# Optimization experiments

Hardware: AMD Instinct MI355X
Metric: run time of the kernel (lower is better)

The kernel has to match this reference:

```python
import jax, jax.numpy as jnp
import numpy as np

B, N, IN_DIM, HID, OUT, HEADS = 2, 1024, 64, 64, 64, 4
PHD1, PHD2 = HID // HEADS, OUT // HEADS
SLOPE = 0.2  # PyG GATv2Conv default negative_slope
EPS = 1e-12  # F.normalize eps


def _gatv2_dense(x, Wl, Wr, att, bias, heads, phd, mask):
    """Dense GATv2 layer over a full adjacency mask.
    x: [B,N,Din]; Wl/Wr: [Din, heads*phd]; att: [heads,phd]; bias: [heads*phd];
    mask: [N,N] bool, mask[i,j]=True means edge j->i exists.
    """
    Bb, Nn, _ = x.shape
    xl = (x @ Wl).reshape(Bb, Nn, heads, phd)  # source features
    xr = (x @ Wr).reshape(Bb, Nn, heads, phd)  # target features
    # s[b,i,j,h,p] = leaky_relu(xr[b,i] + xl[b,j])  (GATv2)
    s = jax.nn.leaky_relu(xr[:, :, None] + xl[:, None, :], SLOPE)
    e = jnp.einsum('bijhp,hp->bijh', s, att)  # [B,Ni,Nj,H]
    e = jnp.where(mask[None, :, :, None], e, -jnp.inf)
    alpha = jax.nn.softmax(e, axis=2)  # softmax over source nodes j
    out = jnp.einsum('bijh,bjhp->bihp', alpha, xl).reshape(Bb, Nn, heads * phd)
    return out + bias


def setup_inputs() -> dict:
    key = jax.random.key(0)
    ks = jax.random.split(key, 10)
    sc = 0.1
    return {
        'x': jax.random.normal(ks[0], (B, N, IN_DIM), jnp.float32),
        'embedding': jax.random.normal(ks[1], (N, HID), jnp.float32),
        'Wl1': jax.random.normal(ks[2], (IN_DIM, HEADS * PHD1), jnp.float32) * sc,
        'Wr1': jax.random.normal(ks[3], (IN_DIM, HEADS * PHD1), jnp.float32) * sc,
        'att1': jax.random.normal(ks[4], (HEADS, PHD1), jnp.float32) * sc,
        'b1': jnp.zeros((HEADS * PHD1,), jnp.float32),
        'Wl2': jax.random.normal(ks[5], (HID, HEADS * PHD2), jnp.float32) * sc,
        'Wr2': jax.random.normal(ks[6], (HID, HEADS * PHD2), jnp.float32) * sc,
        'att2': jax.random.normal(ks[7], (HEADS, PHD2), jnp.float32) * sc,
        'b2': jnp.zeros((HEADS * PHD2,), jnp.float32),
    }


def reference(x, embedding, Wl1, Wr1, att1, b1, Wl2, Wr2, att2, b2):
    # AdaptiveAdjacency: cosine-similarity adjacency; only its nonzero pattern is used.
    norm = jnp.maximum(jnp.linalg.norm(embedding, axis=1, keepdims=True), EPS)
    ne = embedding / norm
    adj = ne @ ne.T  # [N,N]
    # edge set = adj.nonzero(); GATv2Conv(add_self_loops=True) guarantees diagonal
    mask = (adj != 0) | jnp.eye(N, dtype=bool)
    h = jax.nn.relu(_gatv2_dense(x, Wl1, Wr1, att1, b1, HEADS, PHD1, mask))
    # dropout(0.3) in eval mode -> identity
    return _gatv2_dense(h, Wl2, Wr2, att2, b2, HEADS, PHD2, mask)
```

## Files before the change

kernel.cpp:

```cpp
#include <hip/hip_runtime.h>
#include <math.h>

#define NN 1024
#define BB 2
#define D 64
#define NHEAD 4
#define PH 16
#define LOG2E 1.4426950408889634f

template <int CTRL>
__device__ __forceinline__ float dpp_mov(float x) {
    int xi = __builtin_bit_cast(int, x);
    int r = __builtin_amdgcn_update_dpp(0, xi, CTRL, 0xF, 0xF, true);
    return __builtin_bit_cast(float, r);
}

__device__ __forceinline__ float dpp_rowsum16(float t) {
    t += dpp_mov<0x111>(t);
    t += dpp_mov<0x112>(t);
    t += dpp_mov<0x114>(t);
    t += dpp_mov<0x118>(t);
    return t;
}

__device__ __forceinline__ float quad_sum4(float t) {
    t += dpp_mov<0xB1>(t);
    t += dpp_mov<0x4E>(t);
    return t;
}

#define MST 65
__global__ __launch_bounds__(256) void k_mask(const float* __restrict__ emb,
                                              unsigned char* __restrict__ mask) {
    __shared__ float As[64 * MST];
    __shared__ float Bs[64 * MST];
    int tid = threadIdx.x;
    int ib = (blockIdx.x & 15) << 6;
    int jb = (blockIdx.x >> 4) << 6;

    #pragma unroll
    for (int r = 0; r < 4; ++r) {
        int q = tid + (r << 8);
        int row = q >> 4, c4 = (q & 15) << 2;
        float4 a = *(const float4*)&emb[(ib + row) * D + c4];
        float4 b = *(const float4*)&emb[(jb + row) * D + c4];
        As[row * MST + c4 + 0] = a.x; As[row * MST + c4 + 1] = a.y;
        As[row * MST + c4 + 2] = a.z; As[row * MST + c4 + 3] = a.w;
        Bs[row * MST + c4 + 0] = b.x; Bs[row * MST + c4 + 1] = b.y;
        Bs[row * MST + c4 + 2] = b.z; Bs[row * MST + c4 + 3] = b.w;
    }
    __syncthreads();

    int i0 = (tid >> 4) << 2;
    int j0 = (tid & 15) << 2;
    float acc[4][4] = {};
    #pragma unroll 8
    for (int k = 0; k < 64; ++k) {
        float a0 = As[(i0 + 0) * MST + k];
        float a1 = As[(i0 + 1) * MST + k];
        float a2 = As[(i0 + 2) * MST + k];
        float a3 = As[(i0 + 3) * MST + k];
        float b0 = Bs[(j0 + 0) * MST + k];
        float b1 = Bs[(j0 + 1) * MST + k];
        float b2 = Bs[(j0 + 2) * MST + k];
        float b3 = Bs[(j0 + 3) * MST + k];
        acc[0][0] = fmaf(a0, b0, acc[0][0]); acc[0][1] = fmaf(a0, b1, acc[0][1]);
        acc[0][2] = fmaf(a0, b2, acc[0][2]); acc[0][3] = fmaf(a0, b3, acc[0][3]);
        acc[1][0] = fmaf(a1, b0, acc[1][0]); acc[1][1] = fmaf(a1, b1, acc[1][1]);
        acc[1][2] = fmaf(a1, b2, acc[1][2]); acc[1][3] = fmaf(a1, b3, acc[1][3]);
        acc[2][0] = fmaf(a2, b0, acc[2][0]); acc[2][1] = fmaf(a2, b1, acc[2][1]);
        acc[2][2] = fmaf(a2, b2, acc[2][2]); acc[2][3] = fmaf(a2, b3, acc[2][3]);
        acc[3][0] = fmaf(a3, b0, acc[3][0]); acc[3][1] = fmaf(a3, b1, acc[3][1]);
        acc[3][2] = fmaf(a3, b2, acc[3][2]); acc[3][3] = fmaf(a3, b3, acc[3][3]);
    }
    #pragma unroll
    for (int r = 0; r < 4; ++r) {
        int gi = ib + i0 + r;
        uchar4 m;
        m.x = (acc[r][0] != 0.f || gi == jb + j0 + 0) ? 1 : 0;
        m.y = (acc[r][1] != 0.f || gi == jb + j0 + 1) ? 1 : 0;
        m.z = (acc[r][2] != 0.f || gi == jb + j0 + 2) ? 1 : 0;
        m.w = (acc[r][3] != 0.f || gi == jb + j0 + 3) ? 1 : 0;
        *(uchar4*)&mask[gi * NN + jb + j0] = m;
    }
}

__global__ __launch_bounds__(256) void k_gemm2(const float* __restrict__ A,
                                               const float* __restrict__ Wl,
                                               const float* __restrict__ Wr,
                                               const float* __restrict__ att,
                                               float* __restrict__ xl,
                                               float* __restrict__ xr,
                                               float* __restrict__ alE) {
    __shared__ float wl[64 * 64];
    __shared__ float wr[64 * 64];
    int tid = threadIdx.x;
    for (int t = tid; t < 4096; t += 256) { wl[t] = Wl[t]; wr[t] = Wr[t]; }
    __syncthreads();
    int r = blockIdx.x * 4 + (tid >> 6);
    int c = tid & 63;
    float av = att[c];
    const float* arow = A + r * 64;
    float accl = 0.f, accr = 0.f;
    #pragma unroll
    for (int p = 0; p < 64; ++p) {
        float a = arow[p];
        accl = fmaf(a, wl[p * 64 + c], accl);
        accr = fmaf(a, wr[p * 64 + c], accr);
    }
    xl[r * 64 + c] = accl;
    xr[r * 64 + c] = accr;
    float t = dpp_rowsum16(accl * av);
    if ((c & 15) == 15) alE[(r << 2) | (c >> 4)] = 0.6f * LOG2E * t;
}

template <bool RELU>
__global__ __launch_bounds__(256, 4) void k_attn(
    const float* __restrict__ xl, const float* __restrict__ xr,
    const float* __restrict__ att, const float* __restrict__ alE,
    const float* __restrict__ bias, const unsigned char* __restrict__ mask,
    float* __restrict__ out)
{
    __shared__ float Opart[2][4][4][64];
    __shared__ float Lpart[2][4][4][NHEAD];

    int tid = threadIdx.x;
    int wave = tid >> 6, lane = tid & 63;
    int h = lane & 3, jl = lane >> 2;
    int b = blockIdx.x >> 9;
    int i0 = (blockIdx.x & 511) << 1;
    int j0 = (wave << 8) + (jl << 4);

    const float* xlb = xl + (b << 16);

    float at[16], xr0f[16], xr1f[16];
    {
        const float* ap = att + (h << 2);
        const float* r0 = xr + (((b << 10) + i0) << 6) + (h << 2);
        const float* r1 = r0 + 64;
        #pragma unroll
        for (int q = 0; q < 4; ++q) {
            *(float4*)&at[q << 2]   = *(const float4*)(ap + (q << 4));
            *(float4*)&xr0f[q << 2] = *(const float4*)(r0 + (q << 4));
            *(float4*)&xr1f[q << 2] = *(const float4*)(r1 + (q << 4));
        }
        #pragma unroll
        for (int p = 0; p < 16; ++p) at[p] *= 0.4f * LOG2E;
    }
    float ar0q[4], ar1q[4];
    #pragma unroll
    for (int q = 0; q < 4; ++q) {
        float p0 = 0.f, p1 = 0.f;
        #pragma unroll
        for (int r = 0; r < 4; ++r) {
            p0 = fmaf(at[(q << 2) + r], xr0f[(q << 2) + r], p0);
            p1 = fmaf(at[(q << 2) + r], xr1f[(q << 2) + r], p1);
        }
        ar0q[q] = 1.5f * quad_sum4(p0);
        ar1q[q] = 1.5f * quad_sum4(p1);
    }

    unsigned mb0 = 0, mb1 = 0;
    {
        const unsigned* m0p = (const unsigned*)(mask + i0 * NN + j0);
        const unsigned* m1p = (const unsigned*)(mask + (i0 + 1) * NN + j0);
        #pragma unroll
        for (int q = 0; q < 4; ++q) {
            unsigned w0 = m0p[q], w1 = m1p[q];
            mb0 |= ((((w0 >> 0) & 1) | ((w0 >> 7) & 2) | ((w0 >> 14) & 4) | ((w0 >> 21) & 8)) << (q << 2));
            mb1 |= ((((w1 >> 0) & 1) | ((w1 >> 7) & 2) | ((w1 >> 14) & 4) | ((w1 >> 21) & 8)) << (q << 2));
        }
    }

    float O0[16], O1[16], l0q[4] = {}, l1q[4] = {};
    #pragma unroll
    for (int p = 0; p < 16; ++p) { O0[p] = 0.f; O1[p] = 0.f; }

    const float* xrow = xlb + (j0 << 6) + (h << 2);
    const float* alp  = alE + (b << 12) + (j0 << 2);

    #pragma unroll 2
    for (int s = 0; s < 16; ++s) {
        const float* rp = xrow + (s << 6);
        float xv[16];
        *(float4*)&xv[0]  = *(const float4*)(rp);
        *(float4*)&xv[4]  = *(const float4*)(rp + 16);
        *(float4*)&xv[8]  = *(const float4*)(rp + 32);
        *(float4*)&xv[12] = *(const float4*)(rp + 48);
        float alr[4];
        *(float4*)alr = *(const float4*)(alp + (s << 2));
        bool m0 = (mb0 >> s) & 1, m1 = (mb1 >> s) & 1;

        #pragma unroll
        for (int q = 0; q < 4; ++q) {
            float p0 = 0.f, p1 = 0.f;
            #pragma unroll
            for (int r = 0; r < 4; ++r) {
                float xvv = xv[(q << 2) + r];
                float a = at[(q << 2) + r];
                p0 = fmaf(a, __builtin_fabsf(xr0f[(q << 2) + r] + xvv), p0);
                p1 = fmaf(a, __builtin_fabsf(xr1f[(q << 2) + r] + xvv), p1);
            }
            float e0 = quad_sum4(p0) + (ar0q[q] + alr[q]);
            float e1 = quad_sum4(p1) + (ar1q[q] + alr[q]);
            float pe0 = m0 ? __builtin_amdgcn_exp2f(e0) : 0.f;
            float pe1 = m1 ? __builtin_amdgcn_exp2f(e1) : 0.f;
            l0q[q] += pe0;
            l1q[q] += pe1;
            #pragma unroll
            for (int r = 0; r < 4; ++r) {
                float xvv = xv[(q << 2) + r];
                O0[(q << 2) + r] = fmaf(pe0, xvv, O0[(q << 2) + r]);
                O1[(q << 2) + r] = fmaf(pe1, xvv, O1[(q << 2) + r]);
            }
        }
    }

    #pragma unroll
    for (int p = 0; p < 16; ++p) {
        O0[p] += dpp_mov<0x114>(O0[p]);  O0[p] += dpp_mov<0x118>(O0[p]);
        O1[p] += dpp_mov<0x114>(O1[p]);  O1[p] += dpp_mov<0x118>(O1[p]);
    }
    #pragma unroll
    for (int q = 0; q < 4; ++q) {
        l0q[q] += dpp_mov<0x114>(l0q[q]);  l0q[q] += dpp_mov<0x118>(l0q[q]);
        l1q[q] += dpp_mov<0x114>(l1q[q]);  l1q[q] += dpp_mov<0x118>(l1q[q]);
    }

    if ((lane & 15) >= 12) {
        int k = lane >> 4;
        #pragma unroll
        for (int q = 0; q < 4; ++q) {
            *(float4*)&Opart[0][wave][k][(q << 4) + (h << 2)] = *(const float4*)&O0[q << 2];
            *(float4*)&Opart[1][wave][k][(q << 4) + (h << 2)] = *(const float4*)&O1[q << 2];
        }
        if (h == 0) {
            #pragma unroll
            for (int q = 0; q < 4; ++q) {
                Lpart[0][wave][k][q] = l0q[q];
                Lpart[1][wave][k][q] = l1q[q];
            }
        }
    }
    __syncthreads();

    if (tid < 128) {
        int ii = tid >> 6, c = tid & 63;
        float o = 0.f, l = 0.f;
        #pragma unroll
        for (int w = 0; w < 4; ++w)
            #pragma unroll
            for (int k = 0; k < 4; ++k) {
                o += Opart[ii][w][k][c];
                l += Lpart[ii][w][k][c >> 4];
            }
        float res = o / l + bias[c];
        if (RELU) res = fmaxf(res, 0.f);
        out[((b << 10) + i0 + ii) * D + c] = res;
    }
}

extern "C" void kernel_launch(void* const* d_in, const int* in_sizes, int n_in,
                              void* d_out, int out_size, void* d_ws, size_t ws_size,
                              hipStream_t stream) {
    const float* x    = (const float*)d_in[0];
    const float* emb  = (const float*)d_in[1];
    const float* Wl1  = (const float*)d_in[2];
    const float* Wr1  = (const float*)d_in[3];
    const float* att1 = (const float*)d_in[4];
    const float* b1   = (const float*)d_in[5];
    const float* Wl2  = (const float*)d_in[6];
    const float* Wr2  = (const float*)d_in[7];
    const float* att2 = (const float*)d_in[8];
    const float* b2   = (const float*)d_in[9];
    float* out = (float*)d_out;

    unsigned char* mask = (unsigned char*)d_ws;
    float* xl = (float*)(mask + NN * NN);
    float* xr = xl + BB * NN * D;
    float* hbuf = xr + BB * NN * D;
    float* alE = hbuf + BB * NN * D;

    k_mask<<<256, 256, 0, stream>>>(emb, mask);

    k_gemm2<<<BB * NN / 4, 256, 0, stream>>>(x, Wl1, Wr1, att1, xl, xr, alE);
    k_attn<true><<<BB * NN / 2, 256, 0, stream>>>(xl, xr, att1, alE, b1, mask, hbuf);

    k_gemm2<<<BB * NN / 4, 256, 0, stream>>>(hbuf, Wl2, Wr2, att2, xl, xr, alE);
    k_attn<false><<<BB * NN / 2, 256, 0, stream>>>(xl, xr, att2, alE, b2, mask, out);
}
```

Measured before the change: 145.2 us.

## Split attention over source halves and fuse mask, projection, and combine kernels

The attention kernel now splits each target-pair's source range into two halves, doubling block count to 2048 and writing partial numerators and denominators to workspace. New kernels merge the two partials, fusing the layer-1 bias and ReLU with the layer-2 projection, and fusing the mask tile computation with the layer-1 projection. The aim is better occupancy and fewer kernel stages. The cost is extra global traffic for the partials, a separate final combine launch, and a per-row projection that leaves most threads idle and reads weights straight from global memory without shared staging.

```diff
diff --git a/kernel.cpp b/kernel.cpp
--- a/kernel.cpp
+++ b/kernel.cpp
@@ -2,10 +2,6 @@
 #include <math.h>
 
 #define NN 1024
-#define BB 2
-#define D 64
-#define NHEAD 4
-#define PH 16
 #define LOG2E 1.4426950408889634f
 
 template <int CTRL>
@@ -14,7 +10,6 @@
     int r = __builtin_amdgcn_update_dpp(0, xi, CTRL, 0xF, 0xF, true);
     return __builtin_bit_cast(float, r);
 }
-
 __device__ __forceinline__ float dpp_rowsum16(float t) {
     t += dpp_mov<0x111>(t);
     t += dpp_mov<0x112>(t);
@@ -22,117 +17,85 @@
     t += dpp_mov<0x118>(t);
     return t;
 }
-
 __device__ __forceinline__ float quad_sum4(float t) {
     t += dpp_mov<0xB1>(t);
     t += dpp_mov<0x4E>(t);
     return t;
 }
 
-#define MST 65
-__global__ __launch_bounds__(256) void k_mask(const float* __restrict__ emb,
-                                              unsigned char* __restrict__ mask) {
-    __shared__ float As[64 * MST];
-    __shared__ float Bs[64 * MST];
+__device__ void mask_tile(const float* __restrict__ emb,
+                          unsigned char* __restrict__ mask, int task, float* sm) {
+    float* As = sm;
+    float* Bs = sm + 32 * 65;
     int tid = threadIdx.x;
-    int ib = (blockIdx.x & 15) << 6;
-    int jb = (blockIdx.x >> 4) << 6;
-
-    #pragma unroll
-    for (int r = 0; r < 4; ++r) {
+    int ib = (task & 31) << 5;
+    int jb = (task >> 5) << 4;
+    #pragma unroll
+    for (int r = 0; r < 2; ++r) {
         int q = tid + (r << 8);
         int row = q >> 4, c4 = (q & 15) << 2;
-        float4 a = *(const float4*)&emb[(ib + row) * D + c4];
-        float4 b = *(const float4*)&emb[(jb + row) * D + c4];
-        As[row * MST + c4 + 0] = a.x; As[row * MST + c4 + 1] = a.y;
-        As[row * MST + c4 + 2] = a.z; As[row * MST + c4 + 3] = a.w;
-        Bs[row * MST + c4 + 0] = b.x; Bs[row * MST + c4 + 1] = b.y;
-        Bs[row * MST + c4 + 2] = b.z; Bs[row * MST + c4 + 3] = b.w;
+        float4 a = *(const float4*)&emb[(ib + row) * 64 + c4];
+        As[row * 65 + c4 + 0] = a.x; As[row * 65 + c4 + 1] = a.y;
+        As[row * 65 + c4 + 2] = a.z; As[row * 65 + c4 + 3] = a.w;
+    }
+    {
+        int row = tid >> 4, c4 = (tid & 15) << 2;
+        float4 b = *(const float4*)&emb[(jb + row) * 64 + c4];
+        Bs[row * 65 + c4 + 0] = b.x; Bs[row * 65 + c4 + 1] = b.y;
+        Bs[row * 65 + c4 + 2] = b.z; Bs[row * 65 + c4 + 3] = b.w;
     }
     __syncthreads();
-
-    int i0 = (tid >> 4) << 2;
-    int j0 = (tid & 15) << 2;
-    float acc[4][4] = {};
+    int i1 = tid >> 4, j = tid & 15;
+    float acc1 = 0.f, acc2 = 0.f;
     #pragma unroll 8
     for (int k = 0; k < 64; ++k) {
-        float a0 = As[(i0 + 0) * MST + k];
-        float a1 = As[(i0 + 1) * MST + k];
-        float a2 = As[(i0 + 2) * MST + k];
-        float a3 = As[(i0 + 3) * MST + k];
-        float b0 = Bs[(j0 + 0) * MST + k];
-        float b1 = Bs[(j0 + 1) * MST + k];
-        float b2 = Bs[(j0 + 2) * MST + k];
-        float b3 = Bs[(j0 + 3) * MST + k];
-        acc[0][0] = fmaf(a0, b0, acc[0][0]); acc[0][1] = fmaf(a0, b1, acc[0][1]);
-        acc[0][2] = fmaf(a0, b2, acc[0][2]); acc[0][3] = fmaf(a0, b3, acc[0][3]);
-        acc[1][0] = fmaf(a1, b0, acc[1][0]); acc[1][1] = fmaf(a1, b1, acc[1][1]);
-        acc[1][2] = fmaf(a1, b2, acc[1][2]); acc[1][3] = fmaf(a1, b3, acc[1][3]);
-        acc[2][0] = fmaf(a2, b0, acc[2][0]); acc[2][1] = fmaf(a2, b1, acc[2][1]);
-        acc[2][2] = fmaf(a2, b2, acc[2][2]); acc[2][3] = fmaf(a2, b3, acc[2][3]);
-        acc[3][0] = fmaf(a3, b0, acc[3][0]); acc[3][1] = fmaf(a3, b1, acc[3][1]);
-        acc[3][2] = fmaf(a3, b2, acc[3][2]); acc[3][3] = fmaf(a3, b3, acc[3][3]);
-    }
-    #pragma unroll
-    for (int r = 0; r < 4; ++r) {
-        int gi = ib + i0 + r;
-        uchar4 m;
-        m.x = (acc[r][0] != 0.f || gi == jb + j0 + 0) ? 1 : 0;
-        m.y = (acc[r][1] != 0.f || gi == jb + j0 + 1) ? 1 : 0;
-        m.z = (acc[r][2] != 0.f || gi == jb + j0 + 2) ? 1 : 0;
-        m.w = (acc[r][3] != 0.f || gi == jb + j0 + 3) ? 1 : 0;
-        *(uchar4*)&mask[gi * NN + jb + j0] = m;
-    }
-}
-
-__global__ __launch_bounds__(256) void k_gemm2(const float* __restrict__ A,
-                                               const float* __restrict__ Wl,
-                                               const float* __restrict__ Wr,
-                                               const float* __restrict__ att,
-                                               float* __restrict__ xl,
-                                               float* __restrict__ xr,
-                                               float* __restrict__ alE) {
-    __shared__ float wl[64 * 64];
-    __shared__ float wr[64 * 64];
+        float bv = Bs[j * 65 + k];
+        acc1 = fmaf(As[i1 * 65 + k], bv, acc1);
+        acc2 = fmaf(As[(i1 + 16) * 65 + k], bv, acc2);
+    }
+    int gi1 = ib + i1, gi2 = ib + i1 + 16, gj = jb + j;
+    mask[gi1 * NN + gj] = (acc1 != 0.f || gi1 == gj) ? 1 : 0;
+    mask[gi2 * NN + gj] = (acc2 != 0.f || gi2 == gj) ? 1 : 0;
+}
+
+__device__ void gemm_row(const float* __restrict__ Wl, const float* __restrict__ Wr,
+                         const float* __restrict__ att, const float* hrow,
+                         float* __restrict__ xl, float* __restrict__ xr,
+                         float* __restrict__ alE, int r) {
     int tid = threadIdx.x;
-    for (int t = tid; t < 4096; t += 256) { wl[t] = Wl[t]; wr[t] = Wr[t]; }
-    __syncthreads();
-    int r = blockIdx.x * 4 + (tid >> 6);
-    int c = tid & 63;
-    float av = att[c];
-    const float* arow = A + r * 64;
-    float accl = 0.f, accr = 0.f;
-    #pragma unroll
-    for (int p = 0; p < 64; ++p) {
-        float a = arow[p];
-        accl = fmaf(a, wl[p * 64 + c], accl);
-        accr = fmaf(a, wr[p * 64 + c], accr);
-    }
-    xl[r * 64 + c] = accl;
-    xr[r * 64 + c] = accr;
-    float t = dpp_rowsum16(accl * av);
-    if ((c & 15) == 15) alE[(r << 2) | (c >> 4)] = 0.6f * LOG2E * t;
-}
-
-template <bool RELU>
-__global__ __launch_bounds__(256, 4) void k_attn(
-    const float* __restrict__ xl, const float* __restrict__ xr,
-    const float* __restrict__ att, const float* __restrict__ alE,
-    const float* __restrict__ bias, const unsigned char* __restrict__ mask,
-    float* __restrict__ out)
-{
-    __shared__ float Opart[2][4][4][64];
-    __shared__ float Lpart[2][4][4][NHEAD];
-
+    if (tid < 64) {
+        int c = tid;
+        float accl = 0.f, accr = 0.f;
+        #pragma unroll 8
+        for (int p = 0; p < 64; ++p) {
+            float a = hrow[p];
+            accl = fmaf(a, Wl[p * 64 + c], accl);
+            accr = fmaf(a, Wr[p * 64 + c], accr);
+        }
+        xl[r * 64 + c] = accl;
+        xr[r * 64 + c] = accr;
+        float t = dpp_rowsum16(accl * att[c]);
+        if ((c & 15) == 15) alE[(r << 2) | (c >> 4)] = 0.6f * LOG2E * t;
+    }
+}
+
+__device__ void attn_partial(const float* __restrict__ xl, const float* __restrict__ xr,
+                             const float* __restrict__ att, const float* __restrict__ alE,
+                             const unsigned char* __restrict__ mask,
+                             float* __restrict__ Opar, float* __restrict__ lpar,
+                             int task, float* sm) {
+    float* sO = sm;
+    float* sL = sm + 2048;
     int tid = threadIdx.x;
     int wave = tid >> 6, lane = tid & 63;
     int h = lane & 3, jl = lane >> 2;
-    int b = blockIdx.x >> 9;
-    int i0 = (blockIdx.x & 511) << 1;
-    int j0 = (wave << 8) + (jl << 4);
+    int js = task & 1;
+    int p  = task >> 1;
+    int b  = p >> 9;
+    int i0 = (p & 511) << 1;
+    int jbase = (js << 9) + (wave << 7) + (jl << 3);
 
     const float* xlb = xl + (b << 16);
-
     float at[16], xr0f[16], xr1f[16];
     {
         const float* ap = att + (h << 2);
@@ -145,42 +108,38 @@
             *(float4*)&xr1f[q << 2] = *(const float4*)(r1 + (q << 4));
         }
         #pragma unroll
-        for (int p = 0; p < 16; ++p) at[p] *= 0.4f * LOG2E;
+        for (int pp = 0; pp < 16; ++pp) at[pp] *= 0.4f * LOG2E;
     }
     float ar0q[4], ar1q[4];
     #pragma unroll
     for (int q = 0; q < 4; ++q) {
         float p0 = 0.f, p1 = 0.f;
         #pragma unroll
-        for (int r = 0; r < 4; ++r) {
-            p0 = fmaf(at[(q << 2) + r], xr0f[(q << 2) + r], p0);
-            p1 = fmaf(at[(q << 2) + r], xr1f[(q << 2) + r], p1);
+        for (int rr = 0; rr < 4; ++rr) {
+            p0 = fmaf(at[(q << 2) + rr], xr0f[(q << 2) + rr], p0);
+            p1 = fmaf(at[(q << 2) + rr], xr1f[(q << 2) + rr], p1);
         }
         ar0q[q] = 1.5f * quad_sum4(p0);
         ar1q[q] = 1.5f * quad_sum4(p1);
     }
-
     unsigned mb0 = 0, mb1 = 0;
     {
-        const unsigned* m0p = (const unsigned*)(mask + i0 * NN + j0);
-        const unsigned* m1p = (const unsigned*)(mask + (i0 + 1) * NN + j0);
-        #pragma unroll
-        for (int q = 0; q < 4; ++q) {
+        const unsigned* m0p = (const unsigned*)(mask + i0 * NN + jbase);
+        const unsigned* m1p = (const unsigned*)(mask + (i0 + 1) * NN + jbase);
+        #pragma unroll
+        for (int q = 0; q < 2; ++q) {
             unsigned w0 = m0p[q], w1 = m1p[q];
             mb0 |= ((((w0 >> 0) & 1) | ((w0 >> 7) & 2) | ((w0 >> 14) & 4) | ((w0 >> 21) & 8)) << (q << 2));
             mb1 |= ((((w1 >> 0) & 1) | ((w1 >> 7) & 2) | ((w1 >> 14) & 4) | ((w1 >> 21) & 8)) << (q << 2));
         }
     }
-
-    float O0[16], O1[16], l0q[4] = {}, l1q[4] = {};
-    #pragma unroll
-    for (int p = 0; p < 16; ++p) { O0[p] = 0.f; O1[p] = 0.f; }
-
-    const float* xrow = xlb + (j0 << 6) + (h << 2);
-    const float* alp  = alE + (b << 12) + (j0 << 2);
-
+    float O0[16], O1[16], l0q[4] = {0,0,0,0}, l1q[4] = {0,0,0,0};
+    #pragma unroll
+    for (int pp = 0; pp < 16; ++pp) { O0[pp] = 0.f; O1[pp] = 0.f; }
+    const float* xrow = xlb + (jbase << 6) + (h << 2);
+    const float* alp  = alE + (b << 12) + (jbase << 2);
     #pragma unroll 2
-    for (int s = 0; s < 16; ++s) {
+    for (int s = 0; s < 8; ++s) {
         const float* rp = xrow + (s << 6);
         float xv[16];
         *(float4*)&xv[0]  = *(const float4*)(rp);
@@ -190,74 +149,135 @@
         float alr[4];
         *(float4*)alr = *(const float4*)(alp + (s << 2));
         bool m0 = (mb0 >> s) & 1, m1 = (mb1 >> s) & 1;
-
         #pragma unroll
         for (int q = 0; q < 4; ++q) {
             float p0 = 0.f, p1 = 0.f;
             #pragma unroll
-            for (int r = 0; r < 4; ++r) {
-                float xvv = xv[(q << 2) + r];
-                float a = at[(q << 2) + r];
-                p0 = fmaf(a, __builtin_fabsf(xr0f[(q << 2) + r] + xvv), p0);
-                p1 = fmaf(a, __builtin_fabsf(xr1f[(q << 2) + r] + xvv), p1);
+            for (int rr = 0; rr < 4; ++rr) {
+                float xvv = xv[(q << 2) + rr];
+                float a = at[(q << 2) + rr];
+                p0 = fmaf(a, __builtin_fabsf(xr0f[(q << 2) + rr] + xvv), p0);
+                p1 = fmaf(a, __builtin_fabsf(xr1f[(q << 2) + rr] + xvv), p1);
             }
             float e0 = quad_sum4(p0) + (ar0q[q] + alr[q]);
             float e1 = quad_sum4(p1) + (ar1q[q] + alr[q]);
             float pe0 = m0 ? __builtin_amdgcn_exp2f(e0) : 0.f;
             float pe1 = m1 ? __builtin_amdgcn_exp2f(e1) : 0.f;
-            l0q[q] += pe0;
-            l1q[q] += pe1;
+            l0q[q] += pe0; l1q[q] += pe1;
             #pragma unroll
-            for (int r = 0; r < 4; ++r) {
-                float xvv = xv[(q << 2) + r];
-                O0[(q << 2) + r] = fmaf(pe0, xvv, O0[(q << 2) + r]);
-                O1[(q << 2) + r] = fmaf(pe1, xvv, O1[(q << 2) + r]);
+            for (int rr = 0; rr < 4; ++rr) {
+                float xvv = xv[(q << 2) + rr];
+                O0[(q << 2) + rr] = fmaf(pe0, xvv, O0[(q << 2) + rr]);
+                O1[(q << 2) + rr] = fmaf(pe1, xvv, O1[(q << 2) + rr]);
             }
         }
     }
-
-    #pragma unroll
-    for (int p = 0; p < 16; ++p) {
-        O0[p] += dpp_mov<0x114>(O0[p]);  O0[p] += dpp_mov<0x118>(O0[p]);
-        O1[p] += dpp_mov<0x114>(O1[p]);  O1[p] += dpp_mov<0x118>(O1[p]);
+    #pragma unroll
+    for (int pp = 0; pp < 16; ++pp) {
+        O0[pp] += dpp_mov<0x114>(O0[pp]); O0[pp] += dpp_mov<0x118>(O0[pp]);
+        O1[pp] += dpp_mov<0x114>(O1[pp]); O1[pp] += dpp_mov<0x118>(O1[pp]);
     }
     #pragma unroll
     for (int q = 0; q < 4; ++q) {
-        l0q[q] += dpp_mov<0x114>(l0q[q]);  l0q[q] += dpp_mov<0x118>(l0q[q]);
-        l1q[q] += dpp_mov<0x114>(l1q[q]);  l1q[q] += dpp_mov<0x118>(l1q[q]);
-    }
-
+        l0q[q] += dpp_mov<0x114>(l0q[q]); l0q[q] += dpp_mov<0x118>(l0q[q]);
+        l1q[q] += dpp_mov<0x114>(l1q[q]); l1q[q] += dpp_mov<0x118>(l1q[q]);
+    }
     if ((lane & 15) >= 12) {
         int k = lane >> 4;
+        int wk = (wave << 2) + k;
         #pragma unroll
         for (int q = 0; q < 4; ++q) {
-            *(float4*)&Opart[0][wave][k][(q << 4) + (h << 2)] = *(const float4*)&O0[q << 2];
-            *(float4*)&Opart[1][wave][k][(q << 4) + (h << 2)] = *(const float4*)&O1[q << 2];
+            *(float4*)&sO[(wk)      * 64 + (q << 4) + (h << 2)] = *(const float4*)&O0[q << 2];
+            *(float4*)&sO[(16 + wk) * 64 + (q << 4) + (h << 2)] = *(const float4*)&O1[q << 2];
         }
         if (h == 0) {
             #pragma unroll
             for (int q = 0; q < 4; ++q) {
-                Lpart[0][wave][k][q] = l0q[q];
-                Lpart[1][wave][k][q] = l1q[q];
+                sL[(wk << 2) + q]      = l0q[q];
+                sL[64 + (wk << 2) + q] = l1q[q];
             }
         }
     }
     __syncthreads();
-
     if (tid < 128) {
         int ii = tid >> 6, c = tid & 63;
         float o = 0.f, l = 0.f;
         #pragma unroll
-        for (int w = 0; w < 4; ++w)
-            #pragma unroll
-            for (int k = 0; k < 4; ++k) {
-                o += Opart[ii][w][k][c];
-                l += Lpart[ii][w][k][c >> 4];
-            }
-        float res = o / l + bias[c];
-        if (RELU) res = fmaxf(res, 0.f);
-        out[((b << 10) + i0 + ii) * D + c] = res;
-    }
+        for (int wk = 0; wk < 16; ++wk) {
+            o += sO[(ii * 16 + wk) * 64 + c];
+            l += sL[ii * 64 + (wk << 2) + (c >> 4)];
+        }
+        int idx = (((p << 1) | ii) << 1) | js;
+        Opar[(idx << 6) + c] = o;
+        if ((c & 15) == 0) lpar[(idx << 2) + (c >> 4)] = l;
+    }
+}
+
+__device__ __forceinline__ float combine_val(const float* __restrict__ Opar,
+                                             const float* __restrict__ lpar,
+                                             const float* __restrict__ bias,
+                                             int r, int c) {
+    int b = r >> 10, i = r & 1023;
+    int p = (b << 9) | (i >> 1);
+    int ii = i & 1;
+    int base = ((p << 1) | ii) << 1;
+    float o = Opar[(base << 6) + c] + Opar[((base + 1) << 6) + c];
+    float l = lpar[(base << 2) + (c >> 4)] + lpar[((base + 1) << 2) + (c >> 4)];
+    return o / l + bias[c];
+}
+
+__global__ __launch_bounds__(256) void k_p1(const float* __restrict__ x,
+                                            const float* __restrict__ emb,
+                                            const float* __restrict__ Wl1,
+                                            const float* __restrict__ Wr1,
+                                            const float* __restrict__ att1,
+                                            unsigned char* __restrict__ mask,
+                                            float* __restrict__ xl,
+                                            float* __restrict__ xr,
+                                            float* __restrict__ alE) {
+    __shared__ float sm[32 * 65 + 16 * 65];
+    __shared__ float hrow[64];
+    int bid = blockIdx.x;
+    if (threadIdx.x < 64) hrow[threadIdx.x] = x[bid * 64 + threadIdx.x];
+    mask_tile(emb, mask, bid, sm);
+    __syncthreads();
+    gemm_row(Wl1, Wr1, att1, hrow, xl, xr, alE, bid);
+}
+
+__global__ __launch_bounds__(256) void k_attn_f(const float* __restrict__ xl,
+                                                const float* __restrict__ xr,
+                                                const float* __restrict__ att,
+                                                const float* __restrict__ alE,
+                                                const unsigned char* __restrict__ mask,
+                                                float* __restrict__ Opar,
+                                                float* __restrict__ lpar) {
+    __shared__ float sm[2176];
+    attn_partial(xl, xr, att, alE, mask, Opar, lpar, blockIdx.x, sm);
+}
+
+__global__ __launch_bounds__(256) void k_comb_gemm(const float* __restrict__ Opar,
+                                                   const float* __restrict__ lpar,
+                                                   const float* __restrict__ b1,
+                                                   const float* __restrict__ Wl2,
+                                                   const float* __restrict__ Wr2,
+                                                   const float* __restrict__ att2,
+                                                   float* __restrict__ xl,
+                                                   float* __restrict__ xr,
+                                                   float* __restrict__ alE) {
+    __shared__ float hrow[64];
+    int bid = blockIdx.x;
+    if (threadIdx.x < 64)
+        hrow[threadIdx.x] = fmaxf(combine_val(Opar, lpar, b1, bid, threadIdx.x), 0.f);
+    __syncthreads();
+    gemm_row(Wl2, Wr2, att2, hrow, xl, xr, alE, bid);
+}
+
+__global__ __launch_bounds__(64) void k_comb_out(const float* __restrict__ Opar,
+                                                 const float* __restrict__ lpar,
+                                                 const float* __restrict__ b2,
+                                                 float* __restrict__ out) {
+    out[blockIdx.x * 64 + threadIdx.x] =
+        combine_val(Opar, lpar, b2, blockIdx.x, threadIdx.x);
 }
 
 extern "C" void kernel_launch(void* const* d_in, const int* in_sizes, int n_in,
@@ -276,16 +296,15 @@
     float* out = (float*)d_out;
 
     unsigned char* mask = (unsigned char*)d_ws;
-    float* xl = (float*)(mask + NN * NN);
-    float* xr = xl + BB * NN * D;
-    float* hbuf = xr + BB * NN * D;
-    float* alE = hbuf + BB * NN * D;
-
-    k_mask<<<256, 256, 0, stream>>>(emb, mask);
-
-    k_gemm2<<<BB * NN / 4, 256, 0, stream>>>(x, Wl1, Wr1, att1, xl, xr, alE);
-    k_attn<true><<<BB * NN / 2, 256, 0, stream>>>(xl, xr, att1, alE, b1, mask, hbuf);
-
-    k_gemm2<<<BB * NN / 4, 256, 0, stream>>>(hbuf, Wl2, Wr2, att2, xl, xr, alE);
-    k_attn<false><<<BB * NN / 2, 256, 0, stream>>>(xl, xr, att2, alE, b2, mask, out);
-}
+    float* xl   = (float*)(mask + NN * NN);
+    float* xr   = xl + 2 * NN * 64;
+    float* alE  = xr + 2 * NN * 64;
+    float* Opar = alE + 2 * NN * 4;
+    float* lpar = Opar + 1024 * 2 * 2 * 64;
+
+    k_p1<<<2048, 256, 0, stream>>>(x, emb, Wl1, Wr1, att1, mask, xl, xr, alE);
+    k_attn_f<<<2048, 256, 0, stream>>>(xl, xr, att1, alE, mask, Opar, lpar);
+    k_comb_gemm<<<2048, 256, 0, stream>>>(Opar, lpar, b1, Wl2, Wr2, att2, xl, xr, alE);
+    k_attn_f<<<2048, 256, 0, stream>>>(xl, xr, att2, alE, mask, Opar, lpar);
+    k_comb_out<<<2048, 64, 0, stream>>>(Opar, lpar, b2, out);
+}
```

Measured after the change: 149.2 us. 1.03x slower.
